# Kernel optimization log

Measured on AMD Instinct MI355X. Metric: run time of the kernel, lower is better.

The kernel has to match this reference:

```python
import jax, jax.numpy as jnp
import numpy as np

WS = 14
NUM_HEADS = 12


def setup_inputs() -> dict:
    key = jax.random.key(0)
    ks = jax.random.split(key, 5)
    B, H, W, C = 16, 56, 56, 768
    x = jax.random.normal(ks[0], (B, H, W, C), dtype=jnp.float32)
    qkv_w = jax.random.normal(ks[1], (3 * C, C), dtype=jnp.float32) * (C ** -0.5)
    qkv_b = jax.random.normal(ks[2], (3 * C,), dtype=jnp.float32) * 0.02
    proj_w = jax.random.normal(ks[3], (C, C), dtype=jnp.float32) * (C ** -0.5)
    proj_b = jax.random.normal(ks[4], (C,), dtype=jnp.float32) * 0.02
    return {"x": x, "qkv_w": qkv_w, "qkv_b": qkv_b, "proj_w": proj_w, "proj_b": proj_b}


def reference(x, qkv_w, qkv_b, proj_w, proj_b):
    B, H, W, C = x.shape
    ws = WS
    h = NUM_HEADS
    hd = C // h
    scale = hd ** -0.5
    N = ws * ws
    # window partition: (B,H,W,C) -> (B*nw, ws*ws, C)
    xw = x.reshape(B, H // ws, ws, W // ws, ws, C)
    xw = xw.transpose(0, 1, 3, 2, 4, 5).reshape(-1, N, C)
    # qkv projection
    qkv = xw @ qkv_w.T + qkv_b                     # (nwB, N, 3C)
    qkv = qkv.reshape(-1, N, 3, h, hd)
    q, k, v = qkv[:, :, 0], qkv[:, :, 1], qkv[:, :, 2]   # (nwB, N, h, hd)
    attn = jnp.einsum('bnhd,bmhd->bhnm', q, k) * scale   # (nwB, h, N, N)
    attn = jax.nn.softmax(attn, axis=-1)
    o = jnp.einsum('bhnm,bmhd->bnhd', attn, v).reshape(-1, N, C)
    o = o @ proj_w.T + proj_b
    # window unpartition: (B*nw, ws, ws, C) -> (B, H, W, C)
    o = o.reshape(B, H // ws, W // ws, ws, ws, C)
    o = o.transpose(0, 1, 3, 2, 4, 5).reshape(B, H, W, C)
    return o
```

## Files before the change

kernel.cpp:

```cpp
#include <hip/hip_runtime.h>

typedef _Float16 half8 __attribute__((ext_vector_type(8)));
typedef _Float16 half4 __attribute__((ext_vector_type(4)));
typedef float f32x4 __attribute__((ext_vector_type(4)));

#define NTOK 196
#define NHEAD 12

__device__ __forceinline__ ushort f2h_u(float f) {
    _Float16 h = (_Float16)f;
    return __builtin_bit_cast(ushort, h);
}

__device__ __forceinline__ void gl_lds16(const ushort* g, ushort* l) {
    __builtin_amdgcn_global_load_lds((const __attribute__((address_space(1))) void*)g,
                                     (__attribute__((address_space(3))) void*)l,
                                     16, 0, 0);
}

__device__ __forceinline__ int xcd_swz(int bid, int nwg) {
    const int x = bid & 7, o = bid >> 3;
    const int qq = nwg >> 3, rr = nwg & 7;
    return (x < rr ? x * (qq + 1) : rr * (qq + 1) + (x - rr) * qq) + o;
}

__global__ __launch_bounds__(256) void cvt_x(const float* __restrict__ x,
                                             ushort* __restrict__ xb) {
    int idx = blockIdx.x * 256 + threadIdx.x;
    int t   = idx / 192;
    int c   = (idx - t * 192) * 4;
    int win = t / NTOK;
    int n   = t - win * NTOK;
    int b  = win >> 4, wh = (win >> 2) & 3, ww = win & 3;
    int r  = n / 14,  cc = n - r * 14;
    const float4 v = *(const float4*)(x + (((b * 56 + wh * 14 + r) * 56) + ww * 14 + cc) * 768 + c);
    ushort4 o = make_ushort4(f2h_u(v.x), f2h_u(v.y), f2h_u(v.z), f2h_u(v.w));
    *(ushort4*)(xb + t * 768 + c) = o;
}

__global__ __launch_bounds__(256) void cvt_w(const float* __restrict__ qkv_w,
                                             const float* __restrict__ proj_w,
                                             ushort* __restrict__ wq,
                                             ushort* __restrict__ wp) {
    int idx = blockIdx.x * 256 + threadIdx.x;
    int row = idx / 192;
    int c   = (idx - row * 192) * 4;
    const float* src;
    ushort* dst;
    if (row < 2304) { src = qkv_w + row * 768 + c;          dst = wq + row * 768 + c; }
    else            { src = proj_w + (row - 2304) * 768 + c; dst = wp + (row - 2304) * 768 + c; }
    float4 v = *(const float4*)src;
    *(ushort4*)dst = make_ushort4(f2h_u(v.x), f2h_u(v.y), f2h_u(v.z), f2h_u(v.w));
}

__device__ __forceinline__ void kloop256(const ushort* __restrict__ Ab,
                                         const ushort* __restrict__ Bb,
                                         ushort* sh,
                                         f32x4 (&acc)[8][4]) {
    const int tid = threadIdx.x, wave = tid >> 6, lane = tid & 63;
    const int quad = lane >> 4, l16 = lane & 15;
    const int wm = wave >> 2, wn = wave & 3;
    const int sr = lane >> 3;
    const int sc = ((lane & 7) ^ sr) * 8;
    const int rd_xor = (l16 & 7) << 4;
    const int rowB0 = (wn & 1) * 64;
    half8 Ar[4][2], Br[2][2][2];

#define STAGE_Q(srcK, ldsHalf, q) \
    gl_lds16((srcK) + ((q) * 64 + wave * 8 + sr) * 768 + sc, \
             (ldsHalf) + (((q) & 1) * 64 + wave * 8) * 64)

#define LD_A(QM, aB) \
    _Pragma("unroll") for (int mi = 0; mi < 4; ++mi) \
    _Pragma("unroll") for (int kk = 0; kk < 2; ++kk) \
        Ar[mi][kk] = *(const half8*)((aB) + \
            (((((QM) * 64 + mi * 16 + l16) * 128) + kk * 64 + quad * 16) ^ rd_xor))

#define LD_B(QN, bB) \
    _Pragma("unroll") for (int nj = 0; nj < 2; ++nj) \
    _Pragma("unroll") for (int kk = 0; kk < 2; ++kk) \
        Br[QN][nj][kk] = *(const half8*)((bB) + \
            ((((rowB0 + (QN) * 32 + nj * 16 + l16) * 128) + kk * 64 + quad * 16) ^ rd_xor))

#define MFMA_Q(QM, QN) \
    _Pragma("unroll") for (int mi = 0; mi < 4; ++mi) \
    _Pragma("unroll") for (int nj = 0; nj < 2; ++nj) \
    _Pragma("unroll") for (int kk = 0; kk < 2; ++kk) \
        acc[(QM) * 4 + mi][(QN) * 2 + nj] = __builtin_amdgcn_mfma_f32_16x16x32_f16( \
            Ar[mi][kk], Br[QN][nj][kk], acc[(QM) * 4 + mi][(QN) * 2 + nj], 0, 0, 0)

#define PH_SYNC_PRE() do { \
    __builtin_amdgcn_s_barrier(); \
    asm volatile("s_waitcnt lgkmcnt(0)" ::: "memory"); \
    __builtin_amdgcn_sched_barrier(0); \
    __builtin_amdgcn_s_setprio(1); } while (0)

#define PH_SYNC_POST() do { \
    __builtin_amdgcn_s_setprio(0); \
    __builtin_amdgcn_sched_barrier(0); \
    __builtin_amdgcn_s_barrier(); } while (0)

    {
        ushort* a0 = sh;
        ushort* b0 = sh + 32768;
        #pragma unroll
        for (int q = 0; q < 4; ++q) STAGE_Q(Ab, a0 + (q >> 1) * 8192, q);
        #pragma unroll
        for (int q = 0; q < 4; ++q) STAGE_Q(Bb, b0 + (q >> 1) * 8192, q);
        ushort* a1 = sh + 16384;
        ushort* b1 = sh + 32768 + 16384;
        STAGE_Q(Ab + 64, a1, 0);
        STAGE_Q(Ab + 64, a1 + 8192, 2);
        #pragma unroll
        for (int q = 0; q < 4; ++q) STAGE_Q(Bb + 64, b1 + (q >> 1) * 8192, q);
        asm volatile("s_waitcnt vmcnt(6)" ::: "memory");
        __builtin_amdgcn_s_barrier();
    }

    const int NT = 12;
    for (int T = 0; T < NT; ++T) {
        const int buf = T & 1;
        const char* aB = (const char*)(sh + buf * 16384 + wm * 8192);
        const char* bB = (const char*)(sh + 32768 + buf * 16384 + (wn >> 1) * 8192);
        ushort* aN = sh + (buf ^ 1) * 16384;
        ushort* aC = sh + buf * 16384;
        ushort* bC = sh + 32768 + buf * 16384;
        const bool p1 = (T + 1 < NT), p2 = (T + 2 < NT);

        LD_A(0, aB); LD_B(0, bB);
        if (p1) { STAGE_Q(Ab + (T + 1) * 64, aN, 1);
                  STAGE_Q(Ab + (T + 1) * 64, aN + 8192, 3); }
        PH_SYNC_PRE(); MFMA_Q(0, 0); PH_SYNC_POST();

        LD_B(1, bB);
        if (p2) { STAGE_Q(Ab + (T + 2) * 64, aC, 0);
                  STAGE_Q(Ab + (T + 2) * 64, aC + 8192, 2); }
        PH_SYNC_PRE(); MFMA_Q(0, 1); PH_SYNC_POST();

        LD_A(1, aB);
        if (p2) { STAGE_Q(Bb + (T + 2) * 64, bC, 0);
                  STAGE_Q(Bb + (T + 2) * 64, bC, 1); }
        PH_SYNC_PRE(); MFMA_Q(1, 1); PH_SYNC_POST();

        if (p2) { STAGE_Q(Bb + (T + 2) * 64, bC + 8192, 2);
                  STAGE_Q(Bb + (T + 2) * 64, bC + 8192, 3); }
        if (p2)      { asm volatile("s_waitcnt vmcnt(6)" ::: "memory"); }
        else if (p1) { asm volatile("s_waitcnt vmcnt(0)" ::: "memory"); }
        __builtin_amdgcn_s_barrier();
        __builtin_amdgcn_s_setprio(1);
        MFMA_Q(1, 0);
        __builtin_amdgcn_s_setprio(0);
        __builtin_amdgcn_sched_barrier(0);
        __builtin_amdgcn_s_barrier();
    }
#undef STAGE_Q
#undef LD_A
#undef LD_B
#undef MFMA_Q
#undef PH_SYNC_PRE
#undef PH_SYNC_POST
}

__global__ __launch_bounds__(512, 1) void gemm_qkv(const ushort* __restrict__ A,
                                                   const ushort* __restrict__ Wq,
                                                   const float* __restrict__ qkv_b,
                                                   ushort* __restrict__ qbuf,
                                                   ushort* __restrict__ kbuf,
                                                   ushort* __restrict__ vt,
                                                   int MB, int Wc) {
    __shared__ __align__(16) ushort sh[65536];
    const int tid = threadIdx.x, wave = tid >> 6, lane = tid & 63;
    const int quad = lane >> 4, l16 = lane & 15;
    const int wm = wave >> 2, wn = wave & 3;
    const int wg = xcd_swz(blockIdx.x, MB * 9);
    const int mblk = wg / 9, nblk = wg - (wg / 9) * 9;

    f32x4 acc[8][4];
    #pragma unroll
    for (int i = 0; i < 8; ++i)
        #pragma unroll
        for (int j = 0; j < 4; ++j) acc[i][j] = (f32x4){0.f, 0.f, 0.f, 0.f};

    kloop256(A + (size_t)mblk * 256 * 768, Wq + (size_t)nblk * 256 * 768, sh, acc);

    const int sec = nblk / 3;
    const int colq = nblk - sec * 3;
    if (sec != 2) {
        #pragma unroll
        for (int nj = 0; nj < 4; ++nj) {
            const int col_in = colq * 256 + wn * 64 + nj * 16 + l16;
            const float bias = qkv_b[sec * 768 + col_in];
            ushort* dst = (sec == 0) ? qbuf : kbuf;
            #pragma unroll
            for (int mi = 0; mi < 8; ++mi) {
                #pragma unroll
                for (int r = 0; r < 4; ++r) {
                    const int m = mblk * 256 + wm * 128 + mi * 16 + quad * 4 + r;
                    dst[(size_t)m * 768 + col_in] = f2h_u(acc[mi][nj][r] + bias);
                }
            }
        }
    } else {
        const float* bv = qkv_b + 2 * 768;
        #pragma unroll
        for (int p = 0; p < 2; ++p) {
            __syncthreads();
            if (wm == p) {
                #pragma unroll
                for (int nj = 0; nj < 4; ++nj) {
                    const int col = wn * 64 + nj * 16 + l16;
                    const float bias = bv[colq * 256 + col];
                    #pragma unroll
                    for (int mi = 0; mi < 8; ++mi) {
                        #pragma unroll
                        for (int r = 0; r < 4; ++r)
                            sh[col * 132 + mi * 16 + quad * 4 + r] =
                                f2h_u(acc[mi][nj][r] + bias);
                    }
                }
            }
            __syncthreads();
            #pragma unroll
            for (int i = 0; i < 16; ++i) {
                const int ch = i * 512 + tid;
                const int col = ch >> 5, tq = ch & 31;
                const int m = mblk * 256 + p * 128 + tq * 4;
                const int win = m / 196, tok = m - win * 196;
                const int cin = colq * 256 + col;
                const int head = cin >> 6, d = cin & 63;
                *(uint2*)(vt + ((size_t)(head * Wc + win) * 64 + d) * 208 + tok) =
                    *(const uint2*)(sh + col * 132 + tq * 4);
            }
        }
    }
}

__global__ __launch_bounds__(256) void attn(const ushort* __restrict__ qbuf,
                                            const ushort* __restrict__ kbuf,
                                            const ushort* __restrict__ vt,
                                            ushort* __restrict__ ow, int Wc) {
    __shared__ __align__(16) ushort k_s[2 * 208 * 32];
    __shared__ __align__(16) ushort v_t[64 * 216];
    __shared__ __align__(16) ushort pscr[4 * 512];
    const int tid = threadIdx.x, wave = tid >> 6, lane = tid & 63;
    const int quad = lane >> 4, l16 = lane & 15;
    const int head = blockIdx.x % NHEAD, win = blockIdx.x / NHEAD;

    half8 aq0[4], aq1[4];
    #pragma unroll
    for (int si = 0; si < 4; ++si) {
        int strip = wave + si * 4; if (strip > 12) strip = 12;
        int qtok = strip * 16 + l16; if (qtok > 195) qtok = 195;
        const ushort* qp = qbuf + (size_t)(win * NTOK + qtok) * 768 + head * 64 + quad * 8;
        aq0[si] = *(const half8*)qp;
        aq1[si] = *(const half8*)(qp + 32);
    }

    for (int c = tid; c < 1664; c += 256) {
        const int row = c >> 3, c8 = c & 7;
        half8 val = {};
        if (row < NTOK)
            val = *(const half8*)(kbuf + (size_t)(win * NTOK + row) * 768 + head * 64 + c8 * 8);
        *(half8*)(k_s + ((c8 >> 2) * 208 + row) * 32 + (c8 & 3) * 8) = val;
    }
    {
        const ushort* vsrc = vt + (size_t)(head * Wc + win) * 64 * 208;
        for (int c = tid; c < 1664; c += 256) {
            const int d = c / 26, c8 = c - d * 26;
            *(half8*)(v_t + d * 216 + c8 * 8) = *(const half8*)(vsrc + d * 208 + c8 * 8);
        }
    }
    __syncthreads();

    ushort* ps = pscr + wave * 512;
    for (int si = 0; si < 4; ++si) {
        const int strip = wave + si * 4;
        if (strip > 12) break;
        f32x4 sacc[13];
        #pragma unroll
        for (int nt = 0; nt < 13; ++nt) sacc[nt] = (f32x4){0.f, 0.f, 0.f, 0.f};
        #pragma unroll
        for (int nt = 0; nt < 13; ++nt) {
            const int krow = (nt * 16 + l16) * 32 + quad * 8;
            half8 kb0 = *(const half8*)(k_s + krow);
            half8 kb1 = *(const half8*)(k_s + 208 * 32 + krow);
            sacc[nt] = __builtin_amdgcn_mfma_f32_16x16x32_f16(aq0[si], kb0, sacc[nt], 0, 0, 0);
            sacc[nt] = __builtin_amdgcn_mfma_f32_16x16x32_f16(aq1[si], kb1, sacc[nt], 0, 0, 0);
        }
        float P[13][4], linv[4];
        #pragma unroll
        for (int r = 0; r < 4; ++r) {
            float sv[13];
            float mx = -1e30f;
            #pragma unroll
            for (int nt = 0; nt < 13; ++nt) {
                float s = sacc[nt][r] * 0.125f;
                if (nt == 12 && l16 >= 4) s = -1e30f;
                sv[nt] = s;
                mx = fmaxf(mx, s);
            }
            mx = fmaxf(mx, __shfl_xor(mx, 1));
            mx = fmaxf(mx, __shfl_xor(mx, 2));
            mx = fmaxf(mx, __shfl_xor(mx, 4));
            mx = fmaxf(mx, __shfl_xor(mx, 8));
            float l = 0.f;
            #pragma unroll
            for (int nt = 0; nt < 13; ++nt) {
                float e = __expf(sv[nt] - mx);
                P[nt][r] = e;
                l += e;
            }
            l += __shfl_xor(l, 1);
            l += __shfl_xor(l, 2);
            l += __shfl_xor(l, 4);
            l += __shfl_xor(l, 8);
            linv[r] = 1.f / l;
        }
        f32x4 oacc[4];
        #pragma unroll
        for (int dt = 0; dt < 4; ++dt) oacc[dt] = (f32x4){0.f, 0.f, 0.f, 0.f};
        #pragma unroll
        for (int ks = 0; ks < 6; ++ks) {
            #pragma unroll
            for (int h = 0; h < 2; ++h) {
                const int nt = ks * 2 + h;
                #pragma unroll
                for (int r = 0; r < 4; ++r)
                    ps[(quad * 4 + r) * 32 + h * 16 + l16] = f2h_u(P[nt][r]);
            }
            half8 a = *(const half8*)(ps + l16 * 32 + quad * 8);
            #pragma unroll
            for (int dt = 0; dt < 4; ++dt) {
                half8 vb = *(const half8*)(v_t + (dt * 16 + l16) * 216 + ks * 32 + quad * 8);
                oacc[dt] = __builtin_amdgcn_mfma_f32_16x16x32_f16(a, vb, oacc[dt], 0, 0, 0);
            }
        }
        {
            #pragma unroll
            for (int r = 0; r < 4; ++r)
                ps[(quad * 4 + r) * 32 + l16] = f2h_u(P[12][r]);
            half4 a4 = *(const half4*)(ps + l16 * 32 + quad * 4);
            #pragma unroll
            for (int dt = 0; dt < 4; ++dt) {
                half4 vb4 = *(const half4*)(v_t + (dt * 16 + l16) * 216 + 192 + quad * 4);
                oacc[dt] = __builtin_amdgcn_mfma_f32_16x16x16f16(a4, vb4, oacc[dt], 0, 0, 0);
            }
        }
        const int sb = strip * 16;
        #pragma unroll
        for (int r = 0; r < 4; ++r) {
            const int token = sb + quad * 4 + r;
            if (token < NTOK) {
                #pragma unroll
                for (int dt = 0; dt < 4; ++dt)
                    ow[(size_t)(win * NTOK + token) * 768 + head * 64 + dt * 16 + l16] =
                        f2h_u(oacc[dt][r] * linv[r]);
            }
        }
    }
}

__global__ __launch_bounds__(512, 1) void proj_k(const ushort* __restrict__ ow,
                                                 const ushort* __restrict__ wp,
                                                 const float* __restrict__ pb,
                                                 float* __restrict__ out) {
    __shared__ __align__(16) ushort sh[65536];
    const int tid = threadIdx.x, wave = tid >> 6, lane = tid & 63;
    const int quad = lane >> 4, l16 = lane & 15;
    const int wm = wave >> 2, wn = wave & 3;
    const int wg = xcd_swz(blockIdx.x, 196 * 3);
    const int mblk = wg / 3, nblk = wg - (wg / 3) * 3;

    f32x4 acc[8][4];
    #pragma unroll
    for (int i = 0; i < 8; ++i)
        #pragma unroll
        for (int j = 0; j < 4; ++j) acc[i][j] = (f32x4){0.f, 0.f, 0.f, 0.f};

    kloop256(ow + (size_t)mblk * 256 * 768, wp + (size_t)nblk * 256 * 768, sh, acc);

    #pragma unroll
    for (int mi = 0; mi < 8; ++mi) {
        #pragma unroll
        for (int r = 0; r < 4; ++r) {
            int grow = mblk * 256 + wm * 128 + mi * 16 + quad * 4 + r;
            int wnd = grow / 196, tok = grow - wnd * 196;
            int b = wnd >> 4, wh = (wnd >> 2) & 3, ww = wnd & 3;
            int rr = tok / 14, cc = tok - rr * 14;
            float* orow = out + ((b * 56 + wh * 14 + rr) * 56 + ww * 14 + cc) * 768;
            #pragma unroll
            for (int nj = 0; nj < 4; ++nj) {
                int col = nblk * 256 + wn * 64 + nj * 16 + l16;
                orow[col] = acc[mi][nj][r] + pb[col];
            }
        }
    }
}

extern "C" void kernel_launch(void* const* d_in, const int* in_sizes, int n_in,
                              void* d_out, int out_size, void* d_ws, size_t ws_size,
                              hipStream_t stream) {
    const float* x      = (const float*)d_in[0];
    const float* qkv_w  = (const float*)d_in[1];
    const float* qkv_b  = (const float*)d_in[2];
    const float* proj_w = (const float*)d_in[3];
    const float* proj_b = (const float*)d_in[4];
    float* out = (float*)d_out;

    char* ws = (char*)d_ws;
    ushort* xb = (ushort*)ws;
    ushort* wq = (ushort*)(ws + 77070336);
    ushort* wp = (ushort*)(ws + 80609280);
    char* dyn = ws + 81788928;

    size_t avail = ws_size > 81788928u ? ws_size - 81788928u : 0;
    int Wc = 256;
    while (Wc > 64 && (size_t)Wc * 921600u > avail) Wc >>= 1;
    const int nchunk = 256 / Wc;
    const int MB = Wc * NTOK / 256;

    ushort* qbuf = (ushort*)dyn;
    ushort* kbuf = qbuf + (size_t)Wc * NTOK * 768;
    ushort* vt   = kbuf + (size_t)Wc * NTOK * 768;

    cvt_x<<<37632, 256, 0, stream>>>(x, xb);
    cvt_w<<<2304, 256, 0, stream>>>(qkv_w, proj_w, wq, wp);
    hipMemsetAsync(vt, 0, (size_t)Wc * NHEAD * 64 * 208 * 2, stream);

    for (int c = 0; c < nchunk; ++c) {
        const ushort* xbc = xb + (size_t)c * Wc * NTOK * 768;
        ushort* owc = xb + (size_t)c * Wc * NTOK * 768;
        gemm_qkv<<<MB * 9, 512, 0, stream>>>(xbc, wq, qkv_b, qbuf, kbuf, vt, MB, Wc);
        attn<<<Wc * NHEAD, 256, 0, stream>>>(qbuf, kbuf, vt, owc, Wc);
    }
    proj_k<<<196 * 3, 512, 0, stream>>>(xb, wp, proj_b, out);
}
```

Before: 755.9 us.

## Swizzle attention LDS layouts, drop V padding memset, stage projection output via LDS

The attention kernel now stores K and V in compact, unpadded LDS buffers. K and the P scratch use XOR-swizzled addresses to avoid bank conflicts, and the tail MFMA reads only the four real tokens, which removes the memset of the padded V buffer. The projection epilogue writes accumulators plus bias into LDS in 64-row passes, then stores whole output rows with coalesced float4 writes instead of scattered 4-byte stores. The smaller LDS footprint may raise attention occupancy. The epilogue adds extra barriers and LDS round-trips, and correctness now relies on P being zero for the padded tokens so the unzeroed V padding has no effect.

Result: slower. 775.7 us (+2.6%).

```diff
diff --git a/kernel.cpp b/kernel.cpp
--- a/kernel.cpp
+++ b/kernel.cpp
@@ -239,8 +239,8 @@
                                             const ushort* __restrict__ kbuf,
                                             const ushort* __restrict__ vt,
                                             ushort* __restrict__ ow, int Wc) {
-    __shared__ __align__(16) ushort k_s[2 * 208 * 32];
-    __shared__ __align__(16) ushort v_t[64 * 216];
+    __shared__ __align__(16) ushort k_s[196 * 64];
+    __shared__ __align__(16) ushort v_t[64 * 196];
     __shared__ __align__(16) ushort pscr[4 * 512];
     const int tid = threadIdx.x, wave = tid >> 6, lane = tid & 63;
     const int quad = lane >> 4, l16 = lane & 15;
@@ -256,23 +256,22 @@
         aq1[si] = *(const half8*)(qp + 32);
     }
 
-    for (int c = tid; c < 1664; c += 256) {
+    for (int c = tid; c < 1568; c += 256) {
         const int row = c >> 3, c8 = c & 7;
-        half8 val = {};
-        if (row < NTOK)
-            val = *(const half8*)(kbuf + (size_t)(win * NTOK + row) * 768 + head * 64 + c8 * 8);
-        *(half8*)(k_s + ((c8 >> 2) * 208 + row) * 32 + (c8 & 3) * 8) = val;
+        half8 val = *(const half8*)(kbuf + (size_t)(win * NTOK + row) * 768 + head * 64 + c8 * 8);
+        const int wb = (row * 128 + c8 * 16) ^ ((row & 7) << 4);
+        *(half8*)((char*)k_s + wb) = val;
     }
     {
         const ushort* vsrc = vt + (size_t)(head * Wc + win) * 64 * 208;
-        for (int c = tid; c < 1664; c += 256) {
-            const int d = c / 26, c8 = c - d * 26;
-            *(half8*)(v_t + d * 216 + c8 * 8) = *(const half8*)(vsrc + d * 208 + c8 * 8);
+        for (int c = tid; c < 3136; c += 256) {
+            const int d = c / 49, i = c - d * 49;
+            *(uint2*)((char*)v_t + d * 392 + i * 8) = *(const uint2*)(vsrc + d * 208 + i * 4);
         }
     }
     __syncthreads();
 
-    ushort* ps = pscr + wave * 512;
+    char* psb = (char*)(pscr + wave * 512);
     for (int si = 0; si < 4; ++si) {
         const int strip = wave + si * 4;
         if (strip > 12) break;
@@ -281,9 +280,10 @@
         for (int nt = 0; nt < 13; ++nt) sacc[nt] = (f32x4){0.f, 0.f, 0.f, 0.f};
         #pragma unroll
         for (int nt = 0; nt < 13; ++nt) {
-            const int krow = (nt * 16 + l16) * 32 + quad * 8;
-            half8 kb0 = *(const half8*)(k_s + krow);
-            half8 kb1 = *(const half8*)(k_s + 208 * 32 + krow);
+            int krow = nt * 16 + l16; if (krow > 195) krow = 195;
+            const int sw = (krow & 7) << 4;
+            half8 kb0 = *(const half8*)((const char*)k_s + ((krow * 128 + quad * 16) ^ sw));
+            half8 kb1 = *(const half8*)((const char*)k_s + ((krow * 128 + 64 + quad * 16) ^ sw));
             sacc[nt] = __builtin_amdgcn_mfma_f32_16x16x32_f16(aq0[si], kb0, sacc[nt], 0, 0, 0);
             sacc[nt] = __builtin_amdgcn_mfma_f32_16x16x32_f16(aq1[si], kb1, sacc[nt], 0, 0, 0);
         }
@@ -319,30 +319,41 @@
         f32x4 oacc[4];
         #pragma unroll
         for (int dt = 0; dt < 4; ++dt) oacc[dt] = (f32x4){0.f, 0.f, 0.f, 0.f};
+        const int rd_sw = (l16 & 7) << 4;
         #pragma unroll
         for (int ks = 0; ks < 6; ++ks) {
             #pragma unroll
             for (int h = 0; h < 2; ++h) {
                 const int nt = ks * 2 + h;
                 #pragma unroll
-                for (int r = 0; r < 4; ++r)
-                    ps[(quad * 4 + r) * 32 + h * 16 + l16] = f2h_u(P[nt][r]);
-            }
-            half8 a = *(const half8*)(ps + l16 * 32 + quad * 8);
+                for (int r = 0; r < 4; ++r) {
+                    const int row = quad * 4 + r;
+                    *(ushort*)(psb + ((row * 64 + h * 32 + l16 * 2) ^ ((row & 7) << 4))) =
+                        f2h_u(P[nt][r]);
+                }
+            }
+            half8 a = *(const half8*)(psb + ((l16 * 64 + quad * 16) ^ rd_sw));
             #pragma unroll
             for (int dt = 0; dt < 4; ++dt) {
-                half8 vb = *(const half8*)(v_t + (dt * 16 + l16) * 216 + ks * 32 + quad * 8);
+                const char* vrow = (const char*)v_t + (dt * 16 + l16) * 392;
+                half4 lo = *(const half4*)(vrow + ks * 64 + quad * 16);
+                half4 hi = *(const half4*)(vrow + ks * 64 + quad * 16 + 8);
+                half8 vb;
+                #pragma unroll
+                for (int j = 0; j < 4; ++j) { vb[j] = lo[j]; vb[4 + j] = hi[j]; }
                 oacc[dt] = __builtin_amdgcn_mfma_f32_16x16x32_f16(a, vb, oacc[dt], 0, 0, 0);
             }
         }
         {
             #pragma unroll
-            for (int r = 0; r < 4; ++r)
-                ps[(quad * 4 + r) * 32 + l16] = f2h_u(P[12][r]);
-            half4 a4 = *(const half4*)(ps + l16 * 32 + quad * 4);
+            for (int r = 0; r < 4; ++r) {
+                const int row = quad * 4 + r;
+                *(ushort*)(psb + ((row * 64 + l16 * 2) ^ ((row & 7) << 4))) = f2h_u(P[12][r]);
+            }
+            half4 a4 = *(const half4*)(psb + ((l16 * 64 + quad * 8) ^ rd_sw));
             #pragma unroll
             for (int dt = 0; dt < 4; ++dt) {
-                half4 vb4 = *(const half4*)(v_t + (dt * 16 + l16) * 216 + 192 + quad * 4);
+                half4 vb4 = *(const half4*)((const char*)v_t + (dt * 16 + l16) * 392 + 384);
                 oacc[dt] = __builtin_amdgcn_mfma_f32_16x16x16f16(a4, vb4, oacc[dt], 0, 0, 0);
             }
         }
@@ -379,20 +390,37 @@
 
     kloop256(ow + (size_t)mblk * 256 * 768, wp + (size_t)nblk * 256 * 768, sh, acc);
 
+    float* shf = (float*)sh;
     #pragma unroll
-    for (int mi = 0; mi < 8; ++mi) {
-        #pragma unroll
-        for (int r = 0; r < 4; ++r) {
-            int grow = mblk * 256 + wm * 128 + mi * 16 + quad * 4 + r;
-            int wnd = grow / 196, tok = grow - wnd * 196;
-            int b = wnd >> 4, wh = (wnd >> 2) & 3, ww = wnd & 3;
-            int rr = tok / 14, cc = tok - rr * 14;
+    for (int p = 0; p < 4; ++p) {
+        __syncthreads();
+        if (wm == (p >> 1)) {
+            const int mib = (p & 1) * 4;
+            #pragma unroll
+            for (int nj = 0; nj < 4; ++nj) {
+                const int col = wn * 64 + nj * 16 + l16;
+                const float bias = pb[nblk * 256 + col];
+                #pragma unroll
+                for (int mi2 = 0; mi2 < 4; ++mi2) {
+                    #pragma unroll
+                    for (int r = 0; r < 4; ++r)
+                        shf[(mi2 * 16 + quad * 4 + r) * 260 + col] =
+                            acc[mib + mi2][nj][r] + bias;
+                }
+            }
+        }
+        __syncthreads();
+        #pragma unroll
+        for (int it = 0; it < 8; ++it) {
+            const int idx = it * 512 + tid;
+            const int rowL = idx >> 6, c4 = idx & 63;
+            const int grow = mblk * 256 + p * 64 + rowL;
+            const int wnd = grow / 196, tok = grow - wnd * 196;
+            const int b = wnd >> 4, wh = (wnd >> 2) & 3, ww = wnd & 3;
+            const int rr = tok / 14, cc = tok - rr * 14;
             float* orow = out + ((b * 56 + wh * 14 + rr) * 56 + ww * 14 + cc) * 768;
-            #pragma unroll
-            for (int nj = 0; nj < 4; ++nj) {
-                int col = nblk * 256 + wn * 64 + nj * 16 + l16;
-                orow[col] = acc[mi][nj][r] + pb[col];
-            }
+            *(float4*)(orow + nblk * 256 + c4 * 4) =
+                *(const float4*)(shf + rowL * 260 + c4 * 4);
         }
     }
 }
@@ -425,7 +453,6 @@
 
     cvt_x<<<37632, 256, 0, stream>>>(x, xb);
     cvt_w<<<2304, 256, 0, stream>>>(qkv_w, proj_w, wq, wp);
-    hipMemsetAsync(vt, 0, (size_t)Wc * NHEAD * 64 * 208 * 2, stream);
 
     for (int c = 0; c < nchunk; ++c) {
         const ushort* xbc = xb + (size_t)c * Wc * NTOK * 768;
```
